# Kernel tuning notes

Hardware: AMD Instinct MI355X
Metric: run time of the kernel (lower is better)

## Reference

```python
import jax, jax.numpy as jnp
from jax import lax
import numpy as np

L, B, D_IN, D_OUT, D_MLP = 64, 32, 512, 512, 128
WINDOWS = [1, 3]
FEATS = [256, 128]
C = sum(FEATS)  # 384
EPS = 1e-5


def _leaky(x):
    return jnp.where(x >= 0, x, 0.1 * x)


def setup_inputs() -> dict:
    key = jax.random.key(0)
    ks = jax.random.split(key, 16)
    s = lambda k, shp: (jax.random.normal(k, shp, jnp.float32) * 0.02)
    inp = {}
    inp["x"] = jax.random.normal(ks[0], (L, B, D_IN), jnp.float32)
    inp["xs_mask"] = jnp.ones((L, B), jnp.float32)
    # conv + batchnorm params per window
    inp["conv_w0"] = s(ks[1], (FEATS[0], 1, D_IN * WINDOWS[0]))
    inp["conv_b0"] = jnp.zeros((FEATS[0],), jnp.float32)
    inp["gamma0"] = jnp.ones((FEATS[0],), jnp.float32)
    inp["beta0"] = jnp.zeros((FEATS[0],), jnp.float32)
    inp["conv_w1"] = s(ks[2], (FEATS[1], 1, D_IN * WINDOWS[1]))
    inp["conv_b1"] = jnp.zeros((FEATS[1],), jnp.float32)
    inp["gamma1"] = jnp.ones((FEATS[1],), jnp.float32)
    inp["beta1"] = jnp.zeros((FEATS[1],), jnp.float32)
    inp["w0"] = s(ks[3], (2 * C, D_MLP)); inp["b0"] = jnp.zeros((D_MLP,), jnp.float32)
    inp["w1"] = s(ks[4], (D_MLP, D_MLP)); inp["b1"] = jnp.zeros((D_MLP,), jnp.float32)
    inp["w2"] = s(ks[5], (D_MLP, D_MLP)); inp["b2"] = jnp.zeros((D_MLP,), jnp.float32)
    inp["w3"] = s(ks[6], (D_MLP, D_MLP)); inp["b3"] = jnp.zeros((D_MLP,), jnp.float32)
    # output MLP: Linear(d_mlp->d_mlp), Linear(d_mlp->d_out)
    inp["w4"] = s(ks[7], (D_MLP, D_MLP)); inp["b4"] = jnp.zeros((D_MLP,), jnp.float32)
    inp["w5"] = s(ks[8], (D_MLP, D_OUT)); inp["b5"] = jnp.zeros((D_OUT,), jnp.float32)
    return inp


def reference(x, xs_mask, conv_w0, conv_b0, gamma0, beta0, conv_w1, conv_b1,
              gamma1, beta1, w0, b0, w1, b1, w2, b2, w3, b3, w4, b4, w5, b5):
    # x: (L, B, E)
    x = x * xs_mask[:, :, None]
    xf = jnp.transpose(x, (1, 0, 2)).reshape(B, 1, L * D_IN)  # (B, 1, L*E)

    # CNN front-end: Conv1d(stride=d_in) + BatchNorm1d (batch stats) + LeakyReLU
    feats = []
    for win, cw, cb, g, bt in [(WINDOWS[0], conv_w0, conv_b0, gamma0, beta0),
                               (WINDOWS[1], conv_w1, conv_b1, gamma1, beta1)]:
        pad = (win - 1) // 2 * D_IN
        y = lax.conv_general_dilated(xf, cw, window_strides=(D_IN,),
                                     padding=[(pad, pad)],
                                     dimension_numbers=("NCH", "OIH", "NCH"))
        y = y + cb[None, :, None]  # (B, C_k, L)
        m = y.mean(axis=(0, 2))
        v = y.var(axis=(0, 2))  # biased var, as torch BN training mode
        y = (y - m[None, :, None]) / jnp.sqrt(v[None, :, None] + EPS)
        y = y * g[None, :, None] + bt[None, :, None]
        feats.append(_leaky(y))
    h = jnp.concatenate(feats, axis=1)          # (B, C, L)
    h = jnp.transpose(h, (2, 0, 1))             # (L, B, C)
    h = h * xs_mask[:, :, None]

    # Graph propagation: pairwise concat + first linear, split over concat halves
    # cat([h_i, h_j]) @ w0 == h_i @ w0[:C] + h_j @ w0[C:]  (avoids (L,L,B,2C) tensor)
    a = jnp.einsum("lbc,cd->lbd", h, w0[:C])    # (L, B, d_mlp)
    bb = jnp.einsum("lbc,cd->lbd", h, w0[C:])   # (L, B, d_mlp)
    p = _leaky(a[:, None, :, :] + bb[None, :, :, :] + b0)  # (L, L, B, d_mlp)
    p = _leaky(p @ w1 + b1)
    p = _leaky(p @ w2 + b2)
    p = _leaky(p @ w3 + b3)
    p = p * xs_mask[:, None, :, None]
    p = p.mean(axis=1)                          # (L, B, d_mlp)

    out = _leaky(p @ w4 + b4)
    out = _leaky(out @ w5 + b5)                 # (L, B, d_out)
    return out * xs_mask[:, :, None]
```

## Files before the change

### kernel.cpp

```cpp
#include <hip/hip_runtime.h>


#define BB 32
#define CCH 384

__device__ __forceinline__ float leaky(float x) { return fmaxf(x, 0.1f * x); }

typedef _Float16 f16x8 __attribute__((ext_vector_type(8)));
typedef float f32x4 __attribute__((ext_vector_type(4)));

union F8 { uint4 q; f16x8 h; };
union H2 { _Float16 f[2]; uint32_t u; };

__device__ __forceinline__ void split2(float d0, float d1,
                                       uint32_t& hw, uint32_t& lw) {
  H2 h, l;
  h.f[0] = (_Float16)d0; h.f[1] = (_Float16)d1;
  l.f[0] = (_Float16)((d0 - (float)h.f[0]) * 2048.0f);
  l.f[1] = (_Float16)((d1 - (float)h.f[1]) * 2048.0f);
  hw = h.u; lw = l.u;
}

__global__ __launch_bounds__(256) void conv_kernel(
    const float* __restrict__ x, const float* __restrict__ mask,
    const float* __restrict__ cw0, const float* __restrict__ cw1,
    float* __restrict__ yG)
{
  __shared__ float As[32 * 36];
  __shared__ float Ws[32 * 132];
  int bx = blockIdx.x;
  int rt = bx & 63;
  int ct = bx >> 6;
  int row0 = rt * 32;
  int tid = threadIdx.x;

  const float* wbase; int wstride;
  if (ct < 2) { wbase = cw0 + ct * 128 * 512; wstride = 512; }
  else        { wbase = cw1 + (ct - 2) * 512; wstride = 1536; }

  int sr  = tid >> 3;
  int sk4 = (tid & 7) * 4;
  const float* xrow = x + (row0 + sr) * 512;
  float mval = mask[row0 + sr];

  int r4 = (tid >> 5) * 4;
  int c4 = (tid & 31) * 4;

  float acc[4][4] = {{0.f,0.f,0.f,0.f},{0.f,0.f,0.f,0.f},
                     {0.f,0.f,0.f,0.f},{0.f,0.f,0.f,0.f}};
#pragma unroll 1
  for (int k0 = 0; k0 < 512; k0 += 32) {
    float4 xv = *(const float4*)(xrow + k0 + sk4);
    float4 wv[4];
#pragma unroll
    for (int rep = 0; rep < 4; ++rep) {
      int slot = rep * 256 + tid;
      int c = slot >> 3;
      int kq4 = (slot & 7) * 4;
      wv[rep] = *(const float4*)(wbase + c * wstride + k0 + kq4);
    }
    __syncthreads();
    As[(sk4 + 0) * 36 + sr] = xv.x * mval;
    As[(sk4 + 1) * 36 + sr] = xv.y * mval;
    As[(sk4 + 2) * 36 + sr] = xv.z * mval;
    As[(sk4 + 3) * 36 + sr] = xv.w * mval;
#pragma unroll
    for (int rep = 0; rep < 4; ++rep) {
      int slot = rep * 256 + tid;
      int c = slot >> 3;
      int kq4 = (slot & 7) * 4;
      Ws[(kq4 + 0) * 132 + c] = wv[rep].x;
      Ws[(kq4 + 1) * 132 + c] = wv[rep].y;
      Ws[(kq4 + 2) * 132 + c] = wv[rep].z;
      Ws[(kq4 + 3) * 132 + c] = wv[rep].w;
    }
    __syncthreads();
#pragma unroll
    for (int kk = 0; kk < 32; ++kk) {
      float4 a = *(const float4*)&As[kk * 36 + r4];
      float4 w = *(const float4*)&Ws[kk * 132 + c4];
      float av[4] = {a.x, a.y, a.z, a.w};
      float wv2[4] = {w.x, w.y, w.z, w.w};
#pragma unroll
      for (int ri = 0; ri < 4; ++ri)
#pragma unroll
        for (int ci = 0; ci < 4; ++ci)
          acc[ri][ci] = fmaf(av[ri], wv2[ci], acc[ri][ci]);
    }
  }
#pragma unroll
  for (int ci = 0; ci < 4; ++ci)
    *(float4*)&yG[(ct * 128 + c4 + ci) * 2048 + row0 + r4] =
        make_float4(acc[0][ci], acc[1][ci], acc[2][ci], acc[3][ci]);
}

__global__ __launch_bounds__(256) void stats_kernel(
    const float* __restrict__ yG,
    const float* __restrict__ g0, const float* __restrict__ be0,
    const float* __restrict__ g1, const float* __restrict__ be1,
    float* __restrict__ scale, float* __restrict__ shift)
{
  int c = blockIdx.x;
  int tid = threadIdx.x;
  float s = 0.f, s2 = 0.f;
  if (c < 256) {
    const float* src = yG + c * 2048 + tid * 8;
    float4 v0 = *(const float4*)(src);
    float4 v1 = *(const float4*)(src + 4);
    s  = v0.x + v0.y + v0.z + v0.w + v1.x + v1.y + v1.z + v1.w;
    s2 = v0.x*v0.x + v0.y*v0.y + v0.z*v0.z + v0.w*v0.w
       + v1.x*v1.x + v1.y*v1.y + v1.z*v1.z + v1.w*v1.w;
  } else {
    int cc = c - 256;
    const float* p0 = yG + (256 + cc) * 2048;
    const float* p1 = yG + (384 + cc) * 2048;
    const float* p2 = yG + (512 + cc) * 2048;
#pragma unroll
    for (int j = 0; j < 8; ++j) {
      int e = tid * 8 + j;
      float v = p1[e];
      if (e >= 32)   v += p0[e - 32];
      if (e < 2016)  v += p2[e + 32];
      s += v; s2 += v * v;
    }
  }
#pragma unroll
  for (int off = 32; off > 0; off >>= 1) {
    s  += __shfl_down(s, off);
    s2 += __shfl_down(s2, off);
  }
  __shared__ float rs[4], rs2[4];
  int wid = tid >> 6;
  if ((tid & 63) == 0) { rs[wid] = s; rs2[wid] = s2; }
  __syncthreads();
  if (tid == 0) {
    float S  = rs[0] + rs[1] + rs[2] + rs[3];
    float S2 = rs2[0] + rs2[1] + rs2[2] + rs2[3];
    float mean = S * (1.f / 2048.f);
    float var  = S2 * (1.f / 2048.f) - mean * mean;
    float g  = (c < 256) ? g0[c] : g1[c - 256];
    float be = (c < 256) ? be0[c] : be1[c - 256];
    float sc = g / sqrtf(var + 1e-5f);
    scale[c] = sc;
    shift[c] = be - mean * sc;
  }
}

__global__ __launch_bounds__(256) void ab_kernel(
    const float* __restrict__ yG, const float* __restrict__ scale,
    const float* __restrict__ shift, const float* __restrict__ mask,
    const float* __restrict__ w0,
    float* __restrict__ a_arr, float* __restrict__ bb_arr)
{
  __shared__ float As[32 * 36];
  __shared__ float Ws[32 * 68];
  int bx = blockIdx.x;
  int rt = bx & 63, ct = bx >> 6;
  int row0 = rt * 32, n0 = ct * 64;
  int tid = threadIdx.x;
  int r4 = (tid >> 5) * 4;
  int n2 = (tid & 31) * 2;
  int scc = tid >> 3, srr4 = (tid & 7) * 4;
  int wnn8 = (tid & 7) * 8;
  const float* wbase = (n0 < 128) ? (w0 + n0) : (w0 + CCH * 128 + (n0 - 128));
  float4 mv = *(const float4*)(mask + row0 + srr4);

  float acc[4][2] = {{0.f, 0.f}};
#pragma unroll 1
  for (int c0 = 0; c0 < 384; c0 += 32) {
    int c = c0 + scc;
    float4 yv;
    if (c < 256) {
      yv = *(const float4*)(yG + c * 2048 + row0 + srr4);
    } else {
      int cc = c - 256;
      yv = *(const float4*)(yG + (384 + cc) * 2048 + row0 + srr4);
      if (rt > 0) {
        float4 u = *(const float4*)(yG + (256 + cc) * 2048 + row0 + srr4 - 32);
        yv.x += u.x; yv.y += u.y; yv.z += u.z; yv.w += u.w;
      }
      if (rt < 63) {
        float4 u = *(const float4*)(yG + (512 + cc) * 2048 + row0 + srr4 + 32);
        yv.x += u.x; yv.y += u.y; yv.z += u.z; yv.w += u.w;
      }
    }
    float sc = scale[c], sh = shift[c];
    float4 wv0 = *(const float4*)(wbase + c * 128 + wnn8);
    float4 wv1 = *(const float4*)(wbase + c * 128 + wnn8 + 4);
    __syncthreads();
    float4 hv;
    hv.x = leaky(fmaf(yv.x, sc, sh)) * mv.x;
    hv.y = leaky(fmaf(yv.y, sc, sh)) * mv.y;
    hv.z = leaky(fmaf(yv.z, sc, sh)) * mv.z;
    hv.w = leaky(fmaf(yv.w, sc, sh)) * mv.w;
    *(float4*)&As[scc * 36 + srr4] = hv;
    *(float4*)&Ws[scc * 68 + wnn8] = wv0;
    *(float4*)&Ws[scc * 68 + wnn8 + 4] = wv1;
    __syncthreads();
#pragma unroll
    for (int cc = 0; cc < 32; ++cc) {
      float4 a = *(const float4*)&As[cc * 36 + r4];
      float2 w = *(const float2*)&Ws[cc * 68 + n2];
      acc[0][0] = fmaf(a.x, w.x, acc[0][0]); acc[0][1] = fmaf(a.x, w.y, acc[0][1]);
      acc[1][0] = fmaf(a.y, w.x, acc[1][0]); acc[1][1] = fmaf(a.y, w.y, acc[1][1]);
      acc[2][0] = fmaf(a.z, w.x, acc[2][0]); acc[2][1] = fmaf(a.z, w.y, acc[2][1]);
      acc[3][0] = fmaf(a.w, w.x, acc[3][0]); acc[3][1] = fmaf(a.w, w.y, acc[3][1]);
    }
  }
  float* dst; int nd;
  if (n0 < 128) { dst = a_arr; nd = n0; } else { dst = bb_arr; nd = n0 - 128; }
#pragma unroll
  for (int ri = 0; ri < 4; ++ri)
    *(float2*)&dst[(row0 + r4 + ri) * 128 + nd + n2] = make_float2(acc[ri][0], acc[ri][1]);
}

__global__ __launch_bounds__(256) void wsplit_kernel(
    const float* __restrict__ w1, const float* __restrict__ w2,
    const float* __restrict__ w3, uint32_t* __restrict__ wpk)
{
  int e = blockIdx.x * 256 + threadIdx.x;
  int L = e >> 13;
  int r = e & 8191;
  int k2 = r >> 7, n = r & 127;
  int k = k2 * 2;
  const float* w = (L == 0) ? w1 : (L == 1) ? w2 : w3;
  uint32_t hw, lw;
  split2(w[k * 128 + n], w[(k + 1) * 128 + n], hw, lw);
  wpk[L * 8192 + n * 64 + k2] = hw;
  wpk[24576 + L * 8192 + n * 64 + k2] = lw;
}

__global__ __launch_bounds__(512) void pair_kernel(
    const float* __restrict__ a_arr, const float* __restrict__ bb_arr,
    const float* __restrict__ b0, const uint32_t* __restrict__ wpk,
    const float* __restrict__ b1, const float* __restrict__ b2,
    const float* __restrict__ b3,
    const float* __restrict__ mask, float* __restrict__ pmean)
{
  __shared__ uint32_t Ahs[128 * 68];
  __shared__ uint32_t Als[128 * 68];
  int i = blockIdx.x, bp = blockIdx.y;
  int tid = threadIdx.x;

#pragma unroll 1
  for (int it = 0; it < 4; ++it) {
    int idx = it * 512 + tid;
    int r   = idx >> 4;
    int k8  = (idx & 15) * 8;
    int db  = r >> 6, j = r & 63;
    int bq  = bp * 2 + db;
    const float* ap = a_arr + (i * BB + bq) * 128 + k8;
    const float* bbp = bb_arr + (j * BB + bq) * 128 + k8;
    const float* zp = b0 + k8;
    float d[8];
#pragma unroll
    for (int t = 0; t < 8; t += 4) {
      float4 av = *(const float4*)(ap + t);
      float4 bv = *(const float4*)(bbp + t);
      float4 zv = *(const float4*)(zp + t);
      d[t+0] = leaky(av.x + bv.x + zv.x);
      d[t+1] = leaky(av.y + bv.y + zv.y);
      d[t+2] = leaky(av.z + bv.z + zv.z);
      d[t+3] = leaky(av.w + bv.w + zv.w);
    }
    uint4 hq, lq;
    split2(d[0], d[1], hq.x, lq.x);
    split2(d[2], d[3], hq.y, lq.y);
    split2(d[4], d[5], hq.z, lq.z);
    split2(d[6], d[7], hq.w, lq.w);
    *(uint4*)&Ahs[r * 68 + k8 / 2] = hq;
    *(uint4*)&Als[r * 68 + k8 / 2] = lq;
  }
  __syncthreads();

  int wid = __builtin_amdgcn_readfirstlane(tid >> 6);
  int wm = wid & 1, wn = wid >> 1;
  int lane = tid & 63;
  int m16 = lane & 15, q = lane >> 4;

  f32x4 hi[4][2], cr[4][2];

#pragma unroll 1
  for (int L = 0; L < 3; ++L) {
    const uint32_t* WhL = wpk + L * 8192;
    const uint32_t* WlL = wpk + 24576 + L * 8192;
    const float* Bv = (L == 0) ? b1 : (L == 1) ? b2 : b3;
#pragma unroll
    for (int mt = 0; mt < 4; ++mt)
#pragma unroll
      for (int nt = 0; nt < 2; ++nt) {
        hi[mt][nt] = (f32x4){0.f, 0.f, 0.f, 0.f};
        cr[mt][nt] = (f32x4){0.f, 0.f, 0.f, 0.f};
      }

    F8 Wh[2], Wl[2], Whn[2], Wln[2];
#pragma unroll
    for (int nt = 0; nt < 2; ++nt) {
      int wrow = wn * 32 + nt * 16 + m16;
      Wh[nt].q = *(const uint4*)(WhL + wrow * 64 + q * 4);
      Wl[nt].q = *(const uint4*)(WlL + wrow * 64 + q * 4);
    }

#pragma unroll 1
    for (int ks = 0; ks < 4; ++ks) {
      int koff2 = ks * 16 + q * 4;
      if (ks < 3) {
#pragma unroll
        for (int nt = 0; nt < 2; ++nt) {
          int wrow = wn * 32 + nt * 16 + m16;
          Whn[nt].q = *(const uint4*)(WhL + wrow * 64 + koff2 + 16);
          Wln[nt].q = *(const uint4*)(WlL + wrow * 64 + koff2 + 16);
        }
      }
#pragma unroll
      for (int mt = 0; mt < 4; ++mt) {
        int arow = wm * 64 + mt * 16 + m16;
        F8 Ah, Al;
        Ah.q = *(const uint4*)&Ahs[arow * 68 + koff2];
        Al.q = *(const uint4*)&Als[arow * 68 + koff2];
#pragma unroll
        for (int nt = 0; nt < 2; ++nt) {
          hi[mt][nt] = __builtin_amdgcn_mfma_f32_16x16x32_f16(
              Ah.h, Wh[nt].h, hi[mt][nt], 0, 0, 0);
          cr[mt][nt] = __builtin_amdgcn_mfma_f32_16x16x32_f16(
              Ah.h, Wl[nt].h, cr[mt][nt], 0, 0, 0);
          cr[mt][nt] = __builtin_amdgcn_mfma_f32_16x16x32_f16(
              Al.h, Wh[nt].h, cr[mt][nt], 0, 0, 0);
        }
      }
#pragma unroll
      for (int nt = 0; nt < 2; ++nt) { Wh[nt] = Whn[nt]; Wl[nt] = Wln[nt]; }
    }

    float bias[2];
#pragma unroll
    for (int nt = 0; nt < 2; ++nt) bias[nt] = Bv[wn * 32 + nt * 16 + m16];

    if (L < 2) {
      __syncthreads();
      int par = lane & 1;
#pragma unroll
      for (int mt = 0; mt < 4; ++mt)
#pragma unroll
        for (int nt = 0; nt < 2; ++nt) {
          int colw = (wn * 32 + nt * 16 + (m16 & ~1)) >> 1;
#pragma unroll
          for (int rg = 0; rg < 4; ++rg) {
            float d = leaky(hi[mt][nt][rg] + cr[mt][nt][rg] * (1.0f / 2048.0f)
                            + bias[nt]);
            float dn = __shfl_xor(d, 1, 64);
            float de = par ? dn : d;
            float do_ = par ? d : dn;
            uint32_t hw, lw;
            split2(de, do_, hw, lw);
            int row = wm * 64 + mt * 16 + q * 4 + rg;
            if (par) Als[row * 68 + colw] = lw;
            else     Ahs[row * 68 + colw] = hw;
          }
        }
      __syncthreads();
    } else {
      float s[2] = {0.f, 0.f};
#pragma unroll
      for (int nt = 0; nt < 2; ++nt)
#pragma unroll
        for (int mt = 0; mt < 4; ++mt)
#pragma unroll
          for (int rg = 0; rg < 4; ++rg)
            s[nt] += leaky(hi[mt][nt][rg] + cr[mt][nt][rg] * (1.0f / 2048.0f)
                           + bias[nt]);
      int brow = i * BB + bp * 2 + wm;
      float mfac = (1.0f / 64.0f) * mask[brow];
#pragma unroll
      for (int nt = 0; nt < 2; ++nt) {
        s[nt] += __shfl_xor(s[nt], 16, 64);
        s[nt] += __shfl_xor(s[nt], 32, 64);
      }
      if (lane < 16) {
#pragma unroll
        for (int nt = 0; nt < 2; ++nt)
          pmean[brow * 128 + wn * 32 + nt * 16 + m16] = s[nt] * mfac;
      }
    }
  }
}

__global__ __launch_bounds__(256) void out_kernel(
    const float* __restrict__ pmean, const float* __restrict__ w4,
    const float* __restrict__ b4, const float* __restrict__ w5,
    const float* __restrict__ b5, const float* __restrict__ mask,
    float* __restrict__ out)
{
  __shared__ float Pm[16 * 132];
  __shared__ float T4[16 * 132];
  int bx = blockIdx.x;
  int col0 = (bx & 1) * 256;
  int row0 = (bx >> 1) * 16;
  int tid = threadIdx.x;
  int tr = tid >> 4, m = tid & 15;

  {
    const float* src = pmean + (row0 + tr) * 128 + 8 * m;
    *(float4*)&Pm[tr * 132 + 8 * m]     = *(const float4*)(src);
    *(float4*)&Pm[tr * 132 + 8 * m + 4] = *(const float4*)(src + 4);
  }
  __syncthreads();
  {
    int k8 = m * 8;
    float4 bv0 = *(const float4*)(b4 + k8);
    float4 bv1 = *(const float4*)(b4 + k8 + 4);
    float t[8] = {bv0.x, bv0.y, bv0.z, bv0.w, bv1.x, bv1.y, bv1.z, bv1.w};
#pragma unroll 4
    for (int cc = 0; cc < 128; ++cc) {
      float a = Pm[tr * 132 + cc];
      float4 w0v = *(const float4*)(w4 + cc * 128 + k8);
      float4 w1v = *(const float4*)(w4 + cc * 128 + k8 + 4);
      t[0] = fmaf(a, w0v.x, t[0]); t[1] = fmaf(a, w0v.y, t[1]);
      t[2] = fmaf(a, w0v.z, t[2]); t[3] = fmaf(a, w0v.w, t[3]);
      t[4] = fmaf(a, w1v.x, t[4]); t[5] = fmaf(a, w1v.y, t[5]);
      t[6] = fmaf(a, w1v.z, t[6]); t[7] = fmaf(a, w1v.w, t[7]);
    }
    *(float4*)&T4[tr * 132 + k8]     = make_float4(leaky(t[0]), leaky(t[1]), leaky(t[2]), leaky(t[3]));
    *(float4*)&T4[tr * 132 + k8 + 4] = make_float4(leaky(t[4]), leaky(t[5]), leaky(t[6]), leaky(t[7]));
  }
  __syncthreads();
  {
    int c16 = m * 16;
    const float* bsrc = b5 + col0 + c16;
    float o[16];
#pragma unroll
    for (int qq = 0; qq < 4; ++qq) {
      float4 bv = *(const float4*)(bsrc + 4 * qq);
      o[4*qq+0] = bv.x; o[4*qq+1] = bv.y; o[4*qq+2] = bv.z; o[4*qq+3] = bv.w;
    }
#pragma unroll 2
    for (int cc = 0; cc < 128; ++cc) {
      float a = T4[tr * 132 + cc];
      const float* wr = w5 + cc * 512 + col0 + c16;
#pragma unroll
      for (int qq = 0; qq < 4; ++qq) {
        float4 wv = *(const float4*)(wr + 4 * qq);
        o[4*qq+0] = fmaf(a, wv.x, o[4*qq+0]);
        o[4*qq+1] = fmaf(a, wv.y, o[4*qq+1]);
        o[4*qq+2] = fmaf(a, wv.z, o[4*qq+2]);
        o[4*qq+3] = fmaf(a, wv.w, o[4*qq+3]);
      }
    }
    float mv = mask[row0 + tr];
    float* dst = out + (row0 + tr) * 512 + col0 + c16;
#pragma unroll
    for (int qq = 0; qq < 4; ++qq)
      *(float4*)(dst + 4 * qq) = make_float4(leaky(o[4*qq+0]) * mv, leaky(o[4*qq+1]) * mv,
                                             leaky(o[4*qq+2]) * mv, leaky(o[4*qq+3]) * mv);
  }
}

extern "C" void kernel_launch(void* const* d_in, const int* in_sizes, int n_in,
                              void* d_out, int out_size, void* d_ws, size_t ws_size,
                              hipStream_t stream) {
  const float* x    = (const float*)d_in[0];
  const float* mask = (const float*)d_in[1];
  const float* cw0  = (const float*)d_in[2];
  const float* g0   = (const float*)d_in[4];
  const float* be0  = (const float*)d_in[5];
  const float* cw1  = (const float*)d_in[6];
  const float* g1   = (const float*)d_in[8];
  const float* be1  = (const float*)d_in[9];
  const float* w0   = (const float*)d_in[10];
  const float* b0   = (const float*)d_in[11];
  const float* w1   = (const float*)d_in[12];
  const float* b1   = (const float*)d_in[13];
  const float* w2   = (const float*)d_in[14];
  const float* b2   = (const float*)d_in[15];
  const float* w3   = (const float*)d_in[16];
  const float* b3   = (const float*)d_in[17];
  const float* w4   = (const float*)d_in[18];
  const float* b4   = (const float*)d_in[19];
  const float* w5   = (const float*)d_in[20];
  const float* b5   = (const float*)d_in[21];

  float* ws     = (float*)d_ws;
  float* yG     = ws;
  float* pmean  = ws;
  uint32_t* wpk = (uint32_t*)(ws + 262144);
  float* scale  = ws + 1310720;
  float* shift  = ws + 1311104;
  float* a_arr  = ws + 1311488;
  float* bb_arr = ws + 1573632;
  float* outp   = (float*)d_out;

  conv_kernel<<<320, 256, 0, stream>>>(x, mask, cw0, cw1, yG);
  stats_kernel<<<384, 256, 0, stream>>>(yG, g0, be0, g1, be1, scale, shift);
  ab_kernel<<<256, 256, 0, stream>>>(yG, scale, shift, mask, w0, a_arr, bb_arr);
  wsplit_kernel<<<96, 256, 0, stream>>>(w1, w2, w3, wpk);
  dim3 g5(64, 16);
  pair_kernel<<<g5, 512, 0, stream>>>(a_arr, bb_arr, b0, wpk, b1, b2, b3,
                                      mask, pmean);
  out_kernel<<<256, 256, 0, stream>>>(pmean, w4, b4, w5, b5, mask, outp);
}
```

Before: 285.7 us.

## Fuse output MLP into pair kernel and halve pair block to four waves

The pair kernel now runs with 256 threads, so each of its four waves computes a 64x64 output tile (4 N-subtiles) instead of 64x32. This doubles per-wave accumulator registers and W-fragment reuse. The separate out_kernel is removed: the final layer's per-row means are kept in shared memory and the w4/w5 output MLP is computed in the same block for its two rows. This saves a launch and the pmean round trip, but adds serial scalar FMA loops over global weights at the tail of every block and raises register pressure.

```diff
diff --git a/kernel.cpp b/kernel.cpp
--- a/kernel.cpp
+++ b/kernel.cpp
@@ -230,12 +230,14 @@
   wpk[24576 + L * 8192 + n * 64 + k2] = lw;
 }
 
-__global__ __launch_bounds__(512) void pair_kernel(
+__global__ __launch_bounds__(256) void pair_kernel(
     const float* __restrict__ a_arr, const float* __restrict__ bb_arr,
     const float* __restrict__ b0, const uint32_t* __restrict__ wpk,
     const float* __restrict__ b1, const float* __restrict__ b2,
     const float* __restrict__ b3,
-    const float* __restrict__ mask, float* __restrict__ pmean)
+    const float* __restrict__ w4, const float* __restrict__ b4,
+    const float* __restrict__ w5, const float* __restrict__ b5,
+    const float* __restrict__ mask, float* __restrict__ out)
 {
   __shared__ uint32_t Ahs[128 * 68];
   __shared__ uint32_t Als[128 * 68];
@@ -243,8 +245,8 @@
   int tid = threadIdx.x;
 
 #pragma unroll 1
-  for (int it = 0; it < 4; ++it) {
-    int idx = it * 512 + tid;
+  for (int it = 0; it < 8; ++it) {
+    int idx = it * 256 + tid;
     int r   = idx >> 4;
     int k8  = (idx & 15) * 8;
     int db  = r >> 6, j = r & 63;
@@ -278,7 +280,7 @@
   int lane = tid & 63;
   int m16 = lane & 15, q = lane >> 4;
 
-  f32x4 hi[4][2], cr[4][2];
+  f32x4 hi[4][4], cr[4][4];
 
 #pragma unroll 1
   for (int L = 0; L < 3; ++L) {
@@ -288,15 +290,15 @@
 #pragma unroll
     for (int mt = 0; mt < 4; ++mt)
 #pragma unroll
-      for (int nt = 0; nt < 2; ++nt) {
+      for (int nt = 0; nt < 4; ++nt) {
         hi[mt][nt] = (f32x4){0.f, 0.f, 0.f, 0.f};
         cr[mt][nt] = (f32x4){0.f, 0.f, 0.f, 0.f};
       }
 
-    F8 Wh[2], Wl[2], Whn[2], Wln[2];
-#pragma unroll
-    for (int nt = 0; nt < 2; ++nt) {
-      int wrow = wn * 32 + nt * 16 + m16;
+    F8 Wh[4], Wl[4], Whn[4], Wln[4];
+#pragma unroll
+    for (int nt = 0; nt < 4; ++nt) {
+      int wrow = wn * 64 + nt * 16 + m16;
       Wh[nt].q = *(const uint4*)(WhL + wrow * 64 + q * 4);
       Wl[nt].q = *(const uint4*)(WlL + wrow * 64 + q * 4);
     }
@@ -306,8 +308,8 @@
       int koff2 = ks * 16 + q * 4;
       if (ks < 3) {
 #pragma unroll
-        for (int nt = 0; nt < 2; ++nt) {
-          int wrow = wn * 32 + nt * 16 + m16;
+        for (int nt = 0; nt < 4; ++nt) {
+          int wrow = wn * 64 + nt * 16 + m16;
           Whn[nt].q = *(const uint4*)(WhL + wrow * 64 + koff2 + 16);
           Wln[nt].q = *(const uint4*)(WlL + wrow * 64 + koff2 + 16);
         }
@@ -319,7 +321,7 @@
         Ah.q = *(const uint4*)&Ahs[arow * 68 + koff2];
         Al.q = *(const uint4*)&Als[arow * 68 + koff2];
 #pragma unroll
-        for (int nt = 0; nt < 2; ++nt) {
+        for (int nt = 0; nt < 4; ++nt) {
           hi[mt][nt] = __builtin_amdgcn_mfma_f32_16x16x32_f16(
               Ah.h, Wh[nt].h, hi[mt][nt], 0, 0, 0);
           cr[mt][nt] = __builtin_amdgcn_mfma_f32_16x16x32_f16(
@@ -329,12 +331,12 @@
         }
       }
 #pragma unroll
-      for (int nt = 0; nt < 2; ++nt) { Wh[nt] = Whn[nt]; Wl[nt] = Wln[nt]; }
-    }
-
-    float bias[2];
-#pragma unroll
-    for (int nt = 0; nt < 2; ++nt) bias[nt] = Bv[wn * 32 + nt * 16 + m16];
+      for (int nt = 0; nt < 4; ++nt) { Wh[nt] = Whn[nt]; Wl[nt] = Wln[nt]; }
+    }
+
+    float bias[4];
+#pragma unroll
+    for (int nt = 0; nt < 4; ++nt) bias[nt] = Bv[wn * 64 + nt * 16 + m16];
 
     if (L < 2) {
       __syncthreads();
@@ -342,8 +344,8 @@
 #pragma unroll
       for (int mt = 0; mt < 4; ++mt)
 #pragma unroll
-        for (int nt = 0; nt < 2; ++nt) {
-          int colw = (wn * 32 + nt * 16 + (m16 & ~1)) >> 1;
+        for (int nt = 0; nt < 4; ++nt) {
+          int colw = wn * 32 + nt * 8 + (m16 >> 1);
 #pragma unroll
           for (int rg = 0; rg < 4; ++rg) {
             float d = leaky(hi[mt][nt][rg] + cr[mt][nt][rg] * (1.0f / 2048.0f)
@@ -360,98 +362,61 @@
         }
       __syncthreads();
     } else {
-      float s[2] = {0.f, 0.f};
-#pragma unroll
-      for (int nt = 0; nt < 2; ++nt)
+      float s[4] = {0.f, 0.f, 0.f, 0.f};
+#pragma unroll
+      for (int nt = 0; nt < 4; ++nt)
 #pragma unroll
         for (int mt = 0; mt < 4; ++mt)
 #pragma unroll
           for (int rg = 0; rg < 4; ++rg)
             s[nt] += leaky(hi[mt][nt][rg] + cr[mt][nt][rg] * (1.0f / 2048.0f)
                            + bias[nt]);
-      int brow = i * BB + bp * 2 + wm;
-      float mfac = (1.0f / 64.0f) * mask[brow];
-#pragma unroll
-      for (int nt = 0; nt < 2; ++nt) {
+      int browp = i * BB + bp * 2 + wm;
+      float mfac = (1.0f / 64.0f) * mask[browp];
+#pragma unroll
+      for (int nt = 0; nt < 4; ++nt) {
         s[nt] += __shfl_xor(s[nt], 16, 64);
         s[nt] += __shfl_xor(s[nt], 32, 64);
       }
+      __syncthreads();
+      float* Pm = (float*)Ahs;
+      float* T4 = (float*)Ahs + 256;
       if (lane < 16) {
 #pragma unroll
-        for (int nt = 0; nt < 2; ++nt)
-          pmean[brow * 128 + wn * 32 + nt * 16 + m16] = s[nt] * mfac;
-      }
-    }
-  }
-}
-
-__global__ __launch_bounds__(256) void out_kernel(
-    const float* __restrict__ pmean, const float* __restrict__ w4,
-    const float* __restrict__ b4, const float* __restrict__ w5,
-    const float* __restrict__ b5, const float* __restrict__ mask,
-    float* __restrict__ out)
-{
-  __shared__ float Pm[16 * 132];
-  __shared__ float T4[16 * 132];
-  int bx = blockIdx.x;
-  int col0 = (bx & 1) * 256;
-  int row0 = (bx >> 1) * 16;
-  int tid = threadIdx.x;
-  int tr = tid >> 4, m = tid & 15;
-
-  {
-    const float* src = pmean + (row0 + tr) * 128 + 8 * m;
-    *(float4*)&Pm[tr * 132 + 8 * m]     = *(const float4*)(src);
-    *(float4*)&Pm[tr * 132 + 8 * m + 4] = *(const float4*)(src + 4);
-  }
-  __syncthreads();
-  {
-    int k8 = m * 8;
-    float4 bv0 = *(const float4*)(b4 + k8);
-    float4 bv1 = *(const float4*)(b4 + k8 + 4);
-    float t[8] = {bv0.x, bv0.y, bv0.z, bv0.w, bv1.x, bv1.y, bv1.z, bv1.w};
+        for (int nt = 0; nt < 4; ++nt)
+          Pm[wm * 128 + wn * 64 + nt * 16 + m16] = s[nt] * mfac;
+      }
+      __syncthreads();
+      {
+        int row = tid >> 7, k = tid & 127;
+        float t = b4[k];
+#pragma unroll 8
+        for (int c = 0; c < 128; ++c)
+          t = fmaf(Pm[row * 128 + c], w4[c * 128 + k], t);
+        T4[row * 128 + k] = leaky(t);
+      }
+      __syncthreads();
+      {
+        int row = tid >> 7, k = tid & 127;
+        float o0 = b5[k], o1 = b5[k + 128], o2 = b5[k + 256], o3 = b5[k + 384];
 #pragma unroll 4
-    for (int cc = 0; cc < 128; ++cc) {
-      float a = Pm[tr * 132 + cc];
-      float4 w0v = *(const float4*)(w4 + cc * 128 + k8);
-      float4 w1v = *(const float4*)(w4 + cc * 128 + k8 + 4);
-      t[0] = fmaf(a, w0v.x, t[0]); t[1] = fmaf(a, w0v.y, t[1]);
-      t[2] = fmaf(a, w0v.z, t[2]); t[3] = fmaf(a, w0v.w, t[3]);
-      t[4] = fmaf(a, w1v.x, t[4]); t[5] = fmaf(a, w1v.y, t[5]);
-      t[6] = fmaf(a, w1v.z, t[6]); t[7] = fmaf(a, w1v.w, t[7]);
-    }
-    *(float4*)&T4[tr * 132 + k8]     = make_float4(leaky(t[0]), leaky(t[1]), leaky(t[2]), leaky(t[3]));
-    *(float4*)&T4[tr * 132 + k8 + 4] = make_float4(leaky(t[4]), leaky(t[5]), leaky(t[6]), leaky(t[7]));
-  }
-  __syncthreads();
-  {
-    int c16 = m * 16;
-    const float* bsrc = b5 + col0 + c16;
-    float o[16];
-#pragma unroll
-    for (int qq = 0; qq < 4; ++qq) {
-      float4 bv = *(const float4*)(bsrc + 4 * qq);
-      o[4*qq+0] = bv.x; o[4*qq+1] = bv.y; o[4*qq+2] = bv.z; o[4*qq+3] = bv.w;
-    }
-#pragma unroll 2
-    for (int cc = 0; cc < 128; ++cc) {
-      float a = T4[tr * 132 + cc];
-      const float* wr = w5 + cc * 512 + col0 + c16;
-#pragma unroll
-      for (int qq = 0; qq < 4; ++qq) {
-        float4 wv = *(const float4*)(wr + 4 * qq);
-        o[4*qq+0] = fmaf(a, wv.x, o[4*qq+0]);
-        o[4*qq+1] = fmaf(a, wv.y, o[4*qq+1]);
-        o[4*qq+2] = fmaf(a, wv.z, o[4*qq+2]);
-        o[4*qq+3] = fmaf(a, wv.w, o[4*qq+3]);
-      }
-    }
-    float mv = mask[row0 + tr];
-    float* dst = out + (row0 + tr) * 512 + col0 + c16;
-#pragma unroll
-    for (int qq = 0; qq < 4; ++qq)
-      *(float4*)(dst + 4 * qq) = make_float4(leaky(o[4*qq+0]) * mv, leaky(o[4*qq+1]) * mv,
-                                             leaky(o[4*qq+2]) * mv, leaky(o[4*qq+3]) * mv);
+        for (int c = 0; c < 128; ++c) {
+          float a = T4[row * 128 + c];
+          const float* wr = w5 + c * 512;
+          o0 = fmaf(a, wr[k], o0);
+          o1 = fmaf(a, wr[k + 128], o1);
+          o2 = fmaf(a, wr[k + 256], o2);
+          o3 = fmaf(a, wr[k + 384], o3);
+        }
+        int brow = i * BB + bp * 2 + row;
+        float mv = mask[brow];
+        float* dst = out + brow * 512;
+        dst[k]       = leaky(o0) * mv;
+        dst[k + 128] = leaky(o1) * mv;
+        dst[k + 256] = leaky(o2) * mv;
+        dst[k + 384] = leaky(o3) * mv;
+      }
+    }
   }
 }
 
@@ -481,7 +446,6 @@
 
   float* ws     = (float*)d_ws;
   float* yG     = ws;
-  float* pmean  = ws;
   uint32_t* wpk = (uint32_t*)(ws + 262144);
   float* scale  = ws + 1310720;
   float* shift  = ws + 1311104;
@@ -494,7 +458,6 @@
   ab_kernel<<<256, 256, 0, stream>>>(yG, scale, shift, mask, w0, a_arr, bb_arr);
   wsplit_kernel<<<96, 256, 0, stream>>>(w1, w2, w3, wpk);
   dim3 g5(64, 16);
-  pair_kernel<<<g5, 512, 0, stream>>>(a_arr, bb_arr, b0, wpk, b1, b2, b3,
-                                      mask, pmean);
-  out_kernel<<<256, 256, 0, stream>>>(pmean, w4, b4, w5, b5, mask, outp);
-}
+  pair_kernel<<<g5, 256, 0, stream>>>(a_arr, bb_arr, b0, wpk, b1, b2, b3,
+                                      w4, b4, w5, b5, mask, outp);
+}
```

After: 323.3 us. 1.13x slower.
